# Kernel optimization log

Hardware: AMD Instinct MI355X
Metric: run time of the kernel (lower is better)

Reference implementation:

```python
import jax, jax.numpy as jnp
import numpy as np

B, S, L, D = 16, 32, 128, 768
A, T = 10, 5
VOCAB = 1000


def setup_inputs() -> dict:
    key = jax.random.key(0)
    k1, k2, k3, k4, k5 = jax.random.split(key, 5)
    return {
        "sentence_ids": jax.random.randint(k1, (B, S, L), 0, VOCAB, dtype=jnp.int32),
        "sentence_attention_masks": jnp.ones((B, S, L), dtype=jnp.float32),
        "sentence_embeddings": jax.random.normal(k2, (B, S, L, D), dtype=jnp.float32),
        "predicate_ids": jax.random.randint(k3, (B, S, A, T), 0, VOCAB, dtype=jnp.int32),
        "arg0_ids": jax.random.randint(k4, (B, S, A, T), 0, VOCAB, dtype=jnp.int32),
        "arg1_ids": jax.random.randint(k5, (B, S, A, T), 0, VOCAB, dtype=jnp.int32),
    }


def _sentence_mean(emb, masks):
    # emb: [B,S,L,D], masks: [B,S,L] -> [B,S,D]; matches torch masked mean with count clamp(min=1)
    summed = jnp.einsum('bsld,bsl->bsd', emb, masks)
    counts = jnp.maximum(masks.sum(-1, keepdims=True), 1.0)
    return summed / counts


def _arg_embedding(arg_ids, sentence_ids, emb):
    # Vectorized form of the original quadruple loop.
    # match[b,s,a,t,l]: arg token t equals sentence token l and arg token is nonzero
    match = (sentence_ids[:, :, None, None, :] == arg_ids[..., None]) & (arg_ids[..., None] != 0)
    mf = match.astype(emb.dtype)
    counts = mf.sum(-1)                                        # [B,S,A,T]
    # mean embedding over matched sentence positions, per arg token
    avg = jnp.einsum('bsatl,bsld->bsatd', mf, emb) / jnp.maximum(counts, 1.0)[..., None]
    valid = counts > 0                                          # token nonzero AND >=1 match
    # original overwrites with each successive matching token -> keep LAST valid token's avg
    t_len = arg_ids.shape[-1]
    last_t = t_len - 1 - jnp.argmax(valid[..., ::-1], axis=-1)  # [B,S,A]
    has_any = valid.any(-1)                                     # [B,S,A]
    sel = jnp.take_along_axis(avg, last_t[..., None, None], axis=3)[:, :, :, 0, :]  # [B,S,A,D]
    return jnp.where(has_any[..., None], sel, 0.0)


def reference(sentence_ids, sentence_attention_masks, sentence_embeddings,
              predicate_ids, arg0_ids, arg1_ids):
    sent_avg = _sentence_mean(sentence_embeddings, sentence_attention_masks)
    pred = _arg_embedding(predicate_ids, sentence_ids, sentence_embeddings)
    a0 = _arg_embedding(arg0_ids, sentence_ids, sentence_embeddings)
    a1 = _arg_embedding(arg1_ids, sentence_ids, sentence_embeddings)
    return (sent_avg, pred, a0, a1)
```

## Files before the change

### kernel.cpp

```cpp
#include <hip/hip_runtime.h>

#define BB 16
#define SS 32
#define LL 128
#define DD 768
#define AA 10
#define TT 5

#define NSLOT (3 * AA)
#define F4PR  (DD / 4)
#define NTHR  768

__global__ __launch_bounds__(NTHR) void srl_kernel(
    const int*   __restrict__ sent_ids,
    const float* __restrict__ masks,
    const float* __restrict__ emb,
    const int*   __restrict__ pred_ids,
    const int*   __restrict__ arg0_ids,
    const int*   __restrict__ arg1_ids,
    float*       __restrict__ out)
{
    __shared__ int      s_ids[LL];
    __shared__ float    s_mask[LL];
    __shared__ unsigned s_tmask[NSLOT * TT][4];
    __shared__ int      s_tcnt[NSLOT * TT];
    __shared__ unsigned s_smask[NSLOT][4];
    __shared__ float    s_sscale[NSLOT];
    __shared__ float    s_minv;
    __shared__ float4   s_red[4][F4PR];

    const int bs  = blockIdx.x;
    const int tid = threadIdx.x;
    const int f4c = tid % F4PR;
    const int rq  = tid / F4PR;

    if (tid < LL) {
        s_ids[tid]  = sent_ids[(size_t)bs * LL + tid];
        s_mask[tid] = masks[(size_t)bs * LL + tid];
    }
    __syncthreads();

    if (tid == 0) {
        float c = 0.0f;
        for (int l = 0; l < LL; ++l) c += s_mask[l];
        s_minv = 1.0f / fmaxf(c, 1.0f);
    }

    if (tid < NSLOT * TT) {
        const int slot = tid / TT;
        const int t    = tid % TT;
        const int type = slot / AA;
        const int a    = slot % AA;
        const int* ap  = (type == 0) ? pred_ids : (type == 1) ? arg0_ids : arg1_ids;
        const int token = ap[((size_t)bs * AA + a) * TT + t];
        unsigned w0 = 0, w1 = 0, w2 = 0, w3 = 0;
        int cnt = 0;
        if (token != 0) {
            #pragma unroll 4
            for (int l = 0; l < LL; ++l) {
                if (s_ids[l] == token) {
                    ++cnt;
                    if      (l < 32) w0 |= 1u << l;
                    else if (l < 64) w1 |= 1u << (l - 32);
                    else if (l < 96) w2 |= 1u << (l - 64);
                    else             w3 |= 1u << (l - 96);
                }
            }
        }
        s_tmask[tid][0] = w0; s_tmask[tid][1] = w1;
        s_tmask[tid][2] = w2; s_tmask[tid][3] = w3;
        s_tcnt[tid] = cnt;
    }
    __syncthreads();

    if (tid < NSLOT) {
        int sel = -1;
        for (int t = TT - 1; t >= 0; --t) {
            if (s_tcnt[tid * TT + t] > 0) { sel = t; break; }
        }
        if (sel >= 0) {
            const int st = tid * TT + sel;
            s_smask[tid][0] = s_tmask[st][0];
            s_smask[tid][1] = s_tmask[st][1];
            s_smask[tid][2] = s_tmask[st][2];
            s_smask[tid][3] = s_tmask[st][3];
            s_sscale[tid]   = 1.0f / (float)s_tcnt[st];
        } else {
            s_smask[tid][0] = s_smask[tid][1] = s_smask[tid][2] = s_smask[tid][3] = 0u;
            s_sscale[tid]   = 0.0f;
        }
    }
    __syncthreads();

    const float4* embt = (const float4*)emb + (size_t)bs * LL * F4PR;
    float4 acc = make_float4(0.f, 0.f, 0.f, 0.f);
    #pragma unroll 4
    for (int l0 = 0; l0 < LL; l0 += 4) {
        const int row = l0 + rq;
        const float m = s_mask[row];
        const float4 v = embt[(size_t)row * F4PR + f4c];
        acc.x += v.x * m; acc.y += v.y * m;
        acc.z += v.z * m; acc.w += v.w * m;
    }
    s_red[rq][f4c] = acc;
    __syncthreads();

    if (tid < F4PR) {
        const float4 p0 = s_red[0][tid], p1 = s_red[1][tid];
        const float4 p2 = s_red[2][tid], p3 = s_red[3][tid];
        const float inv = s_minv;
        float4 r;
        r.x = (p0.x + p1.x + p2.x + p3.x) * inv;
        r.y = (p0.y + p1.y + p2.y + p3.y) * inv;
        r.z = (p0.z + p1.z + p2.z + p3.z) * inv;
        r.w = (p0.w + p1.w + p2.w + p3.w) * inv;
        ((float4*)out)[(size_t)bs * F4PR + tid] = r;
    }

    const size_t O1_4 = (size_t)BB * SS * F4PR;
    const size_t OA_4 = (size_t)BB * SS * AA * F4PR;
    float4* out4 = (float4*)out;

    for (int sb = 0; sb < 32; sb += 4) {
        const int slot = sb + rq;
        if (slot >= NSLOT) continue;
        const int type = slot / AA;
        const int a    = slot % AA;
        const float scale = s_sscale[slot];
        float4 g = make_float4(0.f, 0.f, 0.f, 0.f);
        if (scale != 0.0f) {
            #pragma unroll
            for (int wi = 0; wi < 4; ++wi) {
                unsigned m = s_smask[slot][wi];
                while (m) {
                    const int l = wi * 32 + __builtin_ctz(m);
                    m &= (m - 1);
                    const float4 v = embt[(size_t)l * F4PR + f4c];
                    g.x += v.x; g.y += v.y; g.z += v.z; g.w += v.w;
                }
            }
            g.x *= scale; g.y *= scale; g.z *= scale; g.w *= scale;
        }
        const size_t base4 = O1_4 + (size_t)type * OA_4 + ((size_t)bs * AA + a) * F4PR;
        out4[base4 + f4c] = g;
    }
}

extern "C" void kernel_launch(void* const* d_in, const int* in_sizes, int n_in,
                              void* d_out, int out_size, void* d_ws, size_t ws_size,
                              hipStream_t stream) {
    const int*   sids  = (const int*)d_in[0];
    const float* masks = (const float*)d_in[1];
    const float* emb   = (const float*)d_in[2];
    const int*   pred  = (const int*)d_in[3];
    const int*   a0    = (const int*)d_in[4];
    const int*   a1    = (const int*)d_in[5];
    float* out = (float*)d_out;

    dim3 grid(BB * SS);
    dim3 block(NTHR);
    srl_kernel<<<grid, block, 0, stream>>>(sids, masks, emb, pred, a0, a1, out);
}
```

Before: 317.4 us.

## Split D dimension across three blocks per sentence and merge sync phases

Launches a 2D grid that splits the 768-wide embedding dimension into three chunks, so each block of 256 threads handles a third of the columns and the grid grows from 512 blocks to 1536. The mask-count reduction becomes a wavefront shuffle, and the last-valid-token slot selection is moved after the sentence-mean pass so one barrier is removed. The aim is better occupancy and load balance across CUs, at the cost of each of the three blocks repeating the token-matching bitmask work.

```diff
diff --git a/kernel.cpp b/kernel.cpp
--- a/kernel.cpp
+++ b/kernel.cpp
@@ -7,9 +7,11 @@
 #define AA 10
 #define TT 5
 
-#define NSLOT (3 * AA)
-#define F4PR  (DD / 4)
-#define NTHR  768
+#define NSLOT  (3 * AA)
+#define NSPLIT 3
+#define F4PR   (DD / 4)
+#define CPH    (F4PR / NSPLIT)
+#define NTHR   (4 * CPH)
 
 __global__ __launch_bounds__(NTHR) void srl_kernel(
     const int*   __restrict__ sent_ids,
@@ -27,24 +29,19 @@
     __shared__ unsigned s_smask[NSLOT][4];
     __shared__ float    s_sscale[NSLOT];
     __shared__ float    s_minv;
-    __shared__ float4   s_red[4][F4PR];
+    __shared__ float4   s_red[4][CPH];
 
     const int bs  = blockIdx.x;
+    const int h   = blockIdx.y;
     const int tid = threadIdx.x;
-    const int f4c = tid % F4PR;
-    const int rq  = tid / F4PR;
+    const int f4c = tid & (CPH - 1);
+    const int rq  = tid >> 6;
 
     if (tid < LL) {
-        s_ids[tid]  = sent_ids[(size_t)bs * LL + tid];
-        s_mask[tid] = masks[(size_t)bs * LL + tid];
+        s_ids[tid]  = sent_ids[bs * LL + tid];
+        s_mask[tid] = masks[bs * LL + tid];
     }
     __syncthreads();
-
-    if (tid == 0) {
-        float c = 0.0f;
-        for (int l = 0; l < LL; ++l) c += s_mask[l];
-        s_minv = 1.0f / fmaxf(c, 1.0f);
-    }
 
     if (tid < NSLOT * TT) {
         const int slot = tid / TT;
@@ -52,7 +49,7 @@
         const int type = slot / AA;
         const int a    = slot % AA;
         const int* ap  = (type == 0) ? pred_ids : (type == 1) ? arg0_ids : arg1_ids;
-        const int token = ap[((size_t)bs * AA + a) * TT + t];
+        const int token = ap[(bs * AA + a) * TT + t];
         unsigned w0 = 0, w1 = 0, w2 = 0, w3 = 0;
         int cnt = 0;
         if (token != 0) {
@@ -71,30 +68,10 @@
         s_tmask[tid][2] = w2; s_tmask[tid][3] = w3;
         s_tcnt[tid] = cnt;
     }
-    __syncthreads();
 
-    if (tid < NSLOT) {
-        int sel = -1;
-        for (int t = TT - 1; t >= 0; --t) {
-            if (s_tcnt[tid * TT + t] > 0) { sel = t; break; }
-        }
-        if (sel >= 0) {
-            const int st = tid * TT + sel;
-            s_smask[tid][0] = s_tmask[st][0];
-            s_smask[tid][1] = s_tmask[st][1];
-            s_smask[tid][2] = s_tmask[st][2];
-            s_smask[tid][3] = s_tmask[st][3];
-            s_sscale[tid]   = 1.0f / (float)s_tcnt[st];
-        } else {
-            s_smask[tid][0] = s_smask[tid][1] = s_smask[tid][2] = s_smask[tid][3] = 0u;
-            s_sscale[tid]   = 0.0f;
-        }
-    }
-    __syncthreads();
-
-    const float4* embt = (const float4*)emb + (size_t)bs * LL * F4PR;
+    const float4* embt = (const float4*)emb + (size_t)bs * LL * F4PR + h * CPH;
     float4 acc = make_float4(0.f, 0.f, 0.f, 0.f);
-    #pragma unroll 4
+    #pragma unroll 8
     for (int l0 = 0; l0 < LL; l0 += 4) {
         const int row = l0 + rq;
         const float m = s_mask[row];
@@ -103,9 +80,17 @@
         acc.z += v.z * m; acc.w += v.w * m;
     }
     s_red[rq][f4c] = acc;
+
+    if (tid >= NTHR - 64) {
+        const int lane = tid & 63;
+        float pm = s_mask[lane] + s_mask[lane + 64];
+        #pragma unroll
+        for (int d = 32; d >= 1; d >>= 1) pm += __shfl_down(pm, d);
+        if (lane == 0) s_minv = 1.0f / fmaxf(pm, 1.0f);
+    }
     __syncthreads();
 
-    if (tid < F4PR) {
+    if (tid < CPH) {
         const float4 p0 = s_red[0][tid], p1 = s_red[1][tid];
         const float4 p2 = s_red[2][tid], p3 = s_red[3][tid];
         const float inv = s_minv;
@@ -114,35 +99,55 @@
         r.y = (p0.y + p1.y + p2.y + p3.y) * inv;
         r.z = (p0.z + p1.z + p2.z + p3.z) * inv;
         r.w = (p0.w + p1.w + p2.w + p3.w) * inv;
-        ((float4*)out)[(size_t)bs * F4PR + tid] = r;
+        ((float4*)out)[(size_t)bs * F4PR + h * CPH + tid] = r;
+    } else if (tid >= 64 && tid < 64 + NSLOT) {
+        const int slot = tid - 64;
+        int sel = -1;
+        #pragma unroll
+        for (int t = TT - 1; t >= 0; --t) {
+            if (sel < 0 && s_tcnt[slot * TT + t] > 0) sel = t;
+        }
+        if (sel >= 0) {
+            const int st = slot * TT + sel;
+            s_smask[slot][0] = s_tmask[st][0];
+            s_smask[slot][1] = s_tmask[st][1];
+            s_smask[slot][2] = s_tmask[st][2];
+            s_smask[slot][3] = s_tmask[st][3];
+            s_sscale[slot]   = 1.0f / (float)s_tcnt[st];
+        } else {
+            s_smask[slot][0] = s_smask[slot][1] = s_smask[slot][2] = s_smask[slot][3] = 0u;
+            s_sscale[slot]   = 0.0f;
+        }
     }
+    __syncthreads();
 
     const size_t O1_4 = (size_t)BB * SS * F4PR;
     const size_t OA_4 = (size_t)BB * SS * AA * F4PR;
     float4* out4 = (float4*)out;
 
+    #pragma unroll
     for (int sb = 0; sb < 32; sb += 4) {
         const int slot = sb + rq;
-        if (slot >= NSLOT) continue;
-        const int type = slot / AA;
-        const int a    = slot % AA;
-        const float scale = s_sscale[slot];
-        float4 g = make_float4(0.f, 0.f, 0.f, 0.f);
-        if (scale != 0.0f) {
-            #pragma unroll
-            for (int wi = 0; wi < 4; ++wi) {
-                unsigned m = s_smask[slot][wi];
-                while (m) {
-                    const int l = wi * 32 + __builtin_ctz(m);
-                    m &= (m - 1);
-                    const float4 v = embt[(size_t)l * F4PR + f4c];
-                    g.x += v.x; g.y += v.y; g.z += v.z; g.w += v.w;
+        if (slot < NSLOT) {
+            const int type = slot / AA;
+            const int a    = slot % AA;
+            const float scale = s_sscale[slot];
+            float4 g = make_float4(0.f, 0.f, 0.f, 0.f);
+            if (scale != 0.0f) {
+                #pragma unroll
+                for (int wi = 0; wi < 4; ++wi) {
+                    unsigned m = s_smask[slot][wi];
+                    while (m) {
+                        const int l = (wi << 5) + __builtin_ctz(m);
+                        m &= (m - 1);
+                        const float4 v = embt[(size_t)l * F4PR + f4c];
+                        g.x += v.x; g.y += v.y; g.z += v.z; g.w += v.w;
+                    }
                 }
+                g.x *= scale; g.y *= scale; g.z *= scale; g.w *= scale;
             }
-            g.x *= scale; g.y *= scale; g.z *= scale; g.w *= scale;
+            out4[O1_4 + (size_t)type * OA_4 + ((size_t)bs * AA + a) * F4PR + h * CPH + f4c] = g;
         }
-        const size_t base4 = O1_4 + (size_t)type * OA_4 + ((size_t)bs * AA + a) * F4PR;
-        out4[base4 + f4c] = g;
     }
 }
 
@@ -157,7 +162,7 @@
     const int*   a1    = (const int*)d_in[5];
     float* out = (float*)d_out;
 
-    dim3 grid(BB * SS);
+    dim3 grid(BB * SS, NSPLIT);
     dim3 block(NTHR);
     srl_kernel<<<grid, block, 0, stream>>>(sids, masks, emb, pred, a0, a1, out);
 }
```

Measured after the change: 310.4 us. 2.2% less time.
